# Kernel optimization log

Measured on AMD Instinct MI355X. Metric: run time of the kernel, lower is better.

## Reference

```python
import jax, jax.numpy as jnp
import numpy as np

N, K, D, H, DK, DV, L, E = 16384, 16, 128, 8, 16, 16, 2, 32
DFF = 4 * D
EPS = 1e-5


def _ln(x, g, b):
    mu = jnp.mean(x, axis=-1, keepdims=True)
    var = jnp.var(x, axis=-1, keepdims=True)
    return (x - mu) * jax.lax.rsqrt(var + EPS) * g + b


def setup_inputs() -> dict:
    key = jax.random.key(0)
    ks = jax.random.split(key, 20)
    inp = {
        "node_h": jax.random.normal(ks[0], (N, D), jnp.float32),
        "src_idx": jax.random.randint(ks[1], (N, K), 0, N),
        "edge_feat": jax.random.normal(ks[2], (N, K, E), jnp.float32),
        "t": jax.random.uniform(ks[3], (N, K), jnp.float32),
        "t_now": jnp.ones((1,), jnp.float32),
        # params (linear weights stored [in, out])
        "edge_fc_w": jax.random.normal(ks[4], (E, D), jnp.float32) * (2.0 / (E + D)) ** 0.5,
        "edge_fc_b": jnp.zeros((D,), jnp.float32),
        "basis_freq": jnp.asarray(1.0 / 10 ** np.linspace(0, 9, D), jnp.float32),
        "phase": jax.random.normal(ks[5], (D,), jnp.float32),
        "wq": jax.random.normal(ks[6], (L, D, H * DK), jnp.float32) * np.sqrt(2.0 / (D + DK)),
        "wk": jax.random.normal(ks[7], (L, D, H * DK), jnp.float32) * np.sqrt(2.0 / (D + DK)),
        "wv": jax.random.normal(ks[8], (L, D, H * DV), jnp.float32) * np.sqrt(2.0 / (D + DV)),
        "attn_fc_w": jax.random.normal(ks[9], (L, H * DV, D), jnp.float32) * (2.0 / (H * DV + D)) ** 0.5,
        "attn_fc_b": jnp.zeros((L, D), jnp.float32),
        "attn_ln_g": jnp.ones((L, D), jnp.float32),
        "attn_ln_b": jnp.zeros((L, D), jnp.float32),
        "ffn_w1": jax.random.normal(ks[10], (L, D, DFF), jnp.float32) * (1.0 / D) ** 0.5,
        "ffn_b1": jnp.zeros((L, DFF), jnp.float32),
        "ffn_w2": jax.random.normal(ks[11], (L, DFF, D), jnp.float32) * (1.0 / DFF) ** 0.5,
        "ffn_b2": jnp.zeros((L, D), jnp.float32),
        "ffn_ln_g": jnp.ones((L, D), jnp.float32),
        "ffn_ln_b": jnp.zeros((L, D), jnp.float32),
        "fea2node_w": jax.random.normal(ks[12], (D, D), jnp.float32) * (2.0 / (D + D)) ** 0.5,
        "fea2node_b": jnp.zeros((D,), jnp.float32),
        "final_ln_g": jnp.ones((D,), jnp.float32),
        "final_ln_b": jnp.zeros((D,), jnp.float32),
    }
    return inp


def reference(node_h, src_idx, edge_feat, t, t_now,
              edge_fc_w, edge_fc_b, basis_freq, phase,
              wq, wk, wv, attn_fc_w, attn_fc_b, attn_ln_g, attn_ln_b,
              ffn_w1, ffn_b1, ffn_w2, ffn_b2, ffn_ln_g, ffn_ln_b,
              fea2node_w, fea2node_b, final_ln_g, final_ln_b):
    scale = 1.0 / np.sqrt(DK).astype(np.float32)
    # message_func: gather src features, edge transform, temporal encoding
    t_enc = jnp.cos((t_now[0] - t)[..., None] * basis_freq + phase)        # [N,K,D]
    z = node_h[src_idx] + jax.nn.gelu(edge_feat @ edge_fc_w + edge_fc_b) + t_enc
    # reduce_func: inner_layer transformer blocks over the K-neighbor mailbox
    f = z
    for i in range(L):
        q = (f @ wq[i]).reshape(N, K, H, DK)
        k = (f @ wk[i]).reshape(N, K, H, DK)
        v = (f @ wv[i]).reshape(N, K, H, DV)
        attn = jax.nn.softmax(jnp.einsum('nqhd,nkhd->nhqk', q, k) * scale, axis=-1)
        out = jnp.einsum('nhqk,nkhd->nqhd', attn, v).reshape(N, K, H * DV)
        f = _ln(out @ attn_fc_w[i] + attn_fc_b[i] + f, attn_ln_g[i], attn_ln_b[i])
        hid = jax.nn.relu(f @ ffn_w1[i] + ffn_b1[i])                        # [N,K,4D]
        f = _ln(hid @ ffn_w2[i] + ffn_b2[i] + f, ffn_ln_g[i], ffn_ln_b[i])
    pooled = jnp.mean(f, axis=1)                                            # [N,D]
    out = _ln(jax.nn.gelu(pooled @ fea2node_w + fea2node_b) + node_h,
              final_ln_g, final_ln_b)
    return out
```

## Files before the change

### kernel.cpp

```cpp
#include <hip/hip_runtime.h>

#define NN 16384
#define OFF_EWT 0
#define OFF_WQT 4096
#define OFF_WKT 36864
#define OFF_WVT 69632
#define OFF_AFT 102400
#define OFF_W1T 135168
#define OFF_W2T 266240
#define OFF_F2N 397312
#define TOTAL_W 413696

typedef __attribute__((ext_vector_type(8))) short bf16x8;
typedef __attribute__((ext_vector_type(4))) short bf16x4;
typedef __attribute__((ext_vector_type(4))) float f32x4;

static __device__ __forceinline__ short f2bf(float f) {
  unsigned u = __builtin_bit_cast(unsigned, f);
  u += 0x7fffu + ((u >> 16) & 1u);
  return (short)(u >> 16);
}
static __device__ __forceinline__ float bf2f(short h) {
  unsigned u = ((unsigned)(unsigned short)h) << 16;
  return __builtin_bit_cast(float, u);
}
static __device__ __forceinline__ float gelu_f(float x) {
  float e = __expf(1.5957691216057308f * (x + 0.044715f * x * x * x));
  return x - x / (e + 1.0f);
}
static __device__ __forceinline__ f32x4 mfma16(bf16x8 a, bf16x8 b, f32x4 c) {
  return __builtin_amdgcn_mfma_f32_16x16x32_bf16(a, b, c, 0, 0, 0);
}
#define SWZM(row) (((((row) & 7) << 4)) ^ ((((row) >> 3) & 3) << 5))
static __device__ __forceinline__ int swzb(int row, int col) {
  return row * 256 + ((col * 2) ^ SWZM(row));
}
static __device__ __forceinline__ bf16x8 tile_ld8(const short* base, int row, int col) {
  return *(const bf16x8*)((const char*)base + swzb(row, col));
}
static __device__ __forceinline__ void tile_st16(short* base, int row, int col, short v) {
  *(short*)((char*)base + swzb(row, col)) = v;
}
static __device__ __forceinline__ void stage_w(short* dst, const short* src, int stride,
                                               int w, int lane) {
  #pragma unroll
  for (int it = 0; it < 2; ++it) {
    int dbase = (it * 4 + w) * 1024;
    int d = dbase + lane * 16;
    int row = d >> 8;
    int scolb = (d & 255) ^ SWZM(row);
    const short* sp = src + row * stride + (scolb >> 1);
    __builtin_amdgcn_global_load_lds(
        (const __attribute__((address_space(1))) unsigned int*)sp,
        (__attribute__((address_space(3))) unsigned int*)((char*)dst + dbase),
        16, 0, 0);
  }
}

#define LDS_FENCE() do {                                       \
    asm volatile("s_waitcnt lgkmcnt(0)" ::: "memory");         \
    __builtin_amdgcn_sched_barrier(0);                         \
  } while (0)

#define ISSUE(SRC, STRIDE) stage_w(bn, (SRC), (STRIDE), w, lane)
#define ENDSTEP() do {                                         \
    __syncthreads();                                           \
    short* _t = bc; bc = bn; bn = _t;                          \
  } while (0)

#define LD_FA2() do {                                                     \
    _Pragma("unroll") for (int _s = 0; _s < 4; ++_s) {                    \
      fA0[_s] = tile_ld8(myQ0, li, _s * 32 + lq * 8);                     \
      fA1[_s] = tile_ld8(myQ1, li, _s * 32 + lq * 8);                     \
    }                                                                     \
  } while (0)

#define ST_TILE(T, ACC)                                                   \
  _Pragma("unroll") for (int _c = 0; _c < 8; ++_c)                        \
    _Pragma("unroll") for (int _r = 0; _r < 4; ++_r)                      \
      tile_st16((T), lq * 4 + _r, _c * 16 + li, f2bf((ACC)[_c][_r]));

#define PROJ2D(BB)                                                        \
    f32x4 ga0 = F0, ga1 = F0, gb0 = F0, gb1 = F0;                         \
    _Pragma("unroll") for (int _s = 0; _s < 4; ++_s) {                    \
      int _sc = _s * 32 + lq * 8;                                         \
      bf16x8 _b0 = tile_ld8((BB), 0 + li, _sc);                           \
      bf16x8 _b1 = tile_ld8((BB), 16 + li, _sc);                          \
      ga0 = mfma16(fA0[_s], _b0, ga0); gb0 = mfma16(fA1[_s], _b0, gb0);   \
      ga1 = mfma16(fA0[_s], _b1, ga1); gb1 = mfma16(fA1[_s], _b1, gb1);   \
    }

#define ST2D(D0, D1, CB)                                                  \
    _Pragma("unroll") for (int _r = 0; _r < 4; ++_r) {                    \
      tile_st16((D0), lq * 4 + _r, (CB) * 16 + li, f2bf(ga0[_r]));        \
      tile_st16((D0), lq * 4 + _r, ((CB) + 1) * 16 + li, f2bf(ga1[_r]));  \
      tile_st16((D1), lq * 4 + _r, (CB) * 16 + li, f2bf(gb0[_r]));        \
      tile_st16((D1), lq * 4 + _r, ((CB) + 1) * 16 + li, f2bf(gb1[_r]));  \
    }

#define ACC2D(AR0, AR1, CB, BB)                                           \
    _Pragma("unroll") for (int _s = 0; _s < 4; ++_s) {                    \
      int _sc = _s * 32 + lq * 8;                                         \
      bf16x8 _b0 = tile_ld8((BB), 0 + li, _sc);                           \
      bf16x8 _b1 = tile_ld8((BB), 16 + li, _sc);                          \
      acc0[(CB)] = mfma16(AR0[_s], _b0, acc0[(CB)]);                      \
      acc1[(CB)] = mfma16(AR1[_s], _b0, acc1[(CB)]);                      \
      acc0[(CB) + 1] = mfma16(AR0[_s], _b1, acc0[(CB) + 1]);              \
      acc1[(CB) + 1] = mfma16(AR1[_s], _b1, acc1[(CB) + 1]);              \
    }

#define LAYER_NORM(A, GP, BP) do {                                        \
    float _gg[8], _bb[8];                                                 \
    _Pragma("unroll") for (int _c = 0; _c < 8; ++_c) {                    \
      _gg[_c] = (GP)[_c * 16 + li]; _bb[_c] = (BP)[_c * 16 + li]; }       \
    _Pragma("unroll") for (int _r = 0; _r < 4; ++_r) {                    \
      float _s1 = 0.f, _s2 = 0.f;                                         \
      _Pragma("unroll") for (int _c = 0; _c < 8; ++_c) {                  \
        float _v = (A)[_c][_r]; _s1 += _v; _s2 += _v * _v; }              \
      _Pragma("unroll") for (int _m = 1; _m <= 8; _m <<= 1) {             \
        _s1 += __shfl_xor(_s1, _m, 64); _s2 += __shfl_xor(_s2, _m, 64); } \
      float _mean = _s1 * (1.f / 128.f);                                  \
      float _var = _s2 * (1.f / 128.f) - _mean * _mean;                   \
      float _rstd = rsqrtf(_var + 1e-5f);                                 \
      _Pragma("unroll") for (int _c = 0; _c < 8; ++_c)                    \
        (A)[_c][_r] = ((A)[_c][_r] - _mean) * _rstd * _gg[_c] + _bb[_c];  \
    }                                                                     \
  } while (0)

#define ATTN(MYQ, MYK, VACC, OA) do {                                     \
    f32x4 _st[8];                                                         \
    _Pragma("unroll") for (int _h = 0; _h < 8; ++_h) {                    \
      bf16x8 _ka = B0, _qa = B0;                                          \
      if (lq < 2) {                                                       \
        _ka = tile_ld8((MYK), li, _h * 16 + lq * 8);                      \
        _qa = tile_ld8((MYQ), li, _h * 16 + lq * 8);                      \
      }                                                                   \
      _st[_h] = mfma16(_ka, _qa, F0);                                     \
    }                                                                     \
    LDS_FENCE();                                                          \
    _Pragma("unroll") for (int _c = 0; _c < 8; ++_c) {                    \
      bf16x4 _pk;                                                         \
      _Pragma("unroll") for (int _r = 0; _r < 4; ++_r)                    \
        _pk[_r] = f2bf((VACC)[_c][_r]);                                   \
      *(bf16x4*)((MYK) + (_c * 16 + li) * 16 + lq * 4) = _pk;             \
    }                                                                     \
    LDS_FENCE();                                                          \
    _Pragma("unroll") for (int _h = 0; _h < 8; ++_h) {                    \
      float _p[4]; float _mx = -1e30f;                                    \
      _Pragma("unroll") for (int _r = 0; _r < 4; ++_r) {                  \
        _p[_r] = _st[_h][_r] * 0.25f; _mx = fmaxf(_mx, _p[_r]); }         \
      _mx = fmaxf(_mx, __shfl_xor(_mx, 16, 64));                          \
      _mx = fmaxf(_mx, __shfl_xor(_mx, 32, 64));                          \
      float _sum = 0.f;                                                   \
      _Pragma("unroll") for (int _r = 0; _r < 4; ++_r) {                  \
        _p[_r] = __expf(_p[_r] - _mx); _sum += _p[_r]; }                  \
      _sum += __shfl_xor(_sum, 16, 64);                                   \
      _sum += __shfl_xor(_sum, 32, 64);                                   \
      float _inv = 1.0f / _sum;                                           \
      _Pragma("unroll") for (int _r = 0; _r < 4; ++_r) _p[_r] *= _inv;    \
      bf16x8 _pa;                                                         \
      _Pragma("unroll") for (int _j = 0; _j < 8; ++_j) {                  \
        float _v = __shfl(_p[_j & 3], li + 16 * (2 * lq + (_j >> 2)), 64);\
        _pa[_j] = (lq < 2) ? f2bf(_v) : (short)0;                         \
      }                                                                   \
      bf16x8 _vb = B0;                                                    \
      if (lq < 2) _vb = *(const bf16x8*)((MYK) + (_h * 16 + li) * 16 + lq * 8); \
      f32x4 _o = mfma16(_pa, _vb, F0);                                    \
      _Pragma("unroll") for (int _r = 0; _r < 4; ++_r)                    \
        tile_st16((MYQ), lq * 4 + _r, _h * 16 + li, f2bf(_o[_r]));        \
    }                                                                     \
    LDS_FENCE();                                                          \
    _Pragma("unroll") for (int _s = 0; _s < 4; ++_s)                      \
      (OA)[_s] = tile_ld8((MYQ), li, _s * 32 + lq * 8);                   \
  } while (0)

__global__ void prep_kernel(const float* __restrict__ ew, const float* __restrict__ wq,
                            const float* __restrict__ wk, const float* __restrict__ wv,
                            const float* __restrict__ afc, const float* __restrict__ w1,
                            const float* __restrict__ w2, const float* __restrict__ f2n,
                            short* __restrict__ wsb) {
  int tt = blockIdx.x * 256 + threadIdx.x;
  if (tt >= TOTAL_W) return;
  short v;
  if (tt < OFF_WQT) {
    int u = tt; int row = u >> 5, colr = u & 31;
    v = f2bf(ew[colr * 128 + row]);
  } else if (tt < OFF_WKT) {
    int u = tt - OFF_WQT; int i = u >> 14; u &= 16383; int row = u >> 7, colr = u & 127;
    v = f2bf(wq[i * 16384 + colr * 128 + row]);
  } else if (tt < OFF_WVT) {
    int u = tt - OFF_WKT; int i = u >> 14; u &= 16383; int row = u >> 7, colr = u & 127;
    v = f2bf(wk[i * 16384 + colr * 128 + row]);
  } else if (tt < OFF_AFT) {
    int u = tt - OFF_WVT; int i = u >> 14; u &= 16383; int row = u >> 7, colr = u & 127;
    v = f2bf(wv[i * 16384 + colr * 128 + row]);
  } else if (tt < OFF_W1T) {
    int u = tt - OFF_AFT; int i = u >> 14; u &= 16383; int row = u >> 7, colr = u & 127;
    v = f2bf(afc[i * 16384 + colr * 128 + row]);
  } else if (tt < OFF_W2T) {
    int u = tt - OFF_W1T; int i = u >> 16; u &= 65535; int row = u >> 7, colr = u & 127;
    v = f2bf(w1[i * 65536 + colr * 512 + row]);
  } else if (tt < OFF_F2N) {
    int u = tt - OFF_W2T; int i = u >> 16; u &= 65535; int row = u >> 9, colr = u & 511;
    v = f2bf(w2[i * 65536 + colr * 128 + row]);
  } else {
    int u = tt - OFF_F2N; int row = u >> 7, colr = u & 127;
    v = f2bf(f2n[colr * 128 + row]);
  }
  wsb[tt] = v;
}

__global__ __launch_bounds__(256, 2) void fused_kernel(
    const float* __restrict__ node_h, const int* __restrict__ src_idx,
    const float* __restrict__ edge_feat, const float* __restrict__ t_arr,
    const float* __restrict__ t_now, const float* __restrict__ edge_fc_b,
    const float* __restrict__ basis_freq, const float* __restrict__ phase,
    const float* __restrict__ attn_fc_b, const float* __restrict__ attn_ln_g,
    const float* __restrict__ attn_ln_b, const float* __restrict__ ffn_b1,
    const float* __restrict__ ffn_b2, const float* __restrict__ ffn_ln_g,
    const float* __restrict__ ffn_ln_b, const float* __restrict__ f2n_b,
    const float* __restrict__ fin_g, const float* __restrict__ fin_b,
    const short* __restrict__ wsb, float* __restrict__ out) {
  __shared__ __align__(16) short bufs0[4096];
  __shared__ __align__(16) short bufs1[4096];
  __shared__ __align__(16) short lds_qk[4][8192];

  const int tid = (int)threadIdx.x;
  const int w = tid >> 6, lane = tid & 63, li = lane & 15, lq = lane >> 4;
  const int n0 = (int)blockIdx.x * 8 + w * 2;
  const int n1 = n0 + 1;
  short* myQ0 = lds_qk[w];
  short* myK0 = lds_qk[w] + 2048;
  short* myQ1 = lds_qk[w] + 4096;
  short* myK1 = lds_qk[w] + 6144;
  short* bc = bufs0;
  short* bn = bufs1;
  const f32x4 F0 = {0.f, 0.f, 0.f, 0.f};
  const bf16x8 B0 = {0, 0, 0, 0, 0, 0, 0, 0};

  stage_w(bc, wsb + OFF_WQT, 128, w, lane);

  const float tnow = t_now[0];

  f32x4 acc0[8], acc1[8];
  {
    const short* ewt = wsb + OFF_EWT;
    const float* ef0 = edge_feat + ((size_t)(n0 * 16 + li)) * 32 + lq * 8;
    const float* ef1 = edge_feat + ((size_t)(n1 * 16 + li)) * 32 + lq * 8;
    f32x4 ea0 = *(const f32x4*)(ef0), ea0b = *(const f32x4*)(ef0 + 4);
    f32x4 ea1 = *(const f32x4*)(ef1), ea1b = *(const f32x4*)(ef1 + 4);
    bf16x8 e0, e1;
    #pragma unroll
    for (int j = 0; j < 4; ++j) {
      e0[j] = f2bf(ea0[j]); e0[j + 4] = f2bf(ea0b[j]);
      e1[j] = f2bf(ea1[j]); e1[j + 4] = f2bf(ea1b[j]);
    }
    #pragma unroll
    for (int c = 0; c < 8; ++c) {
      bf16x8 eb = *(const bf16x8*)(ewt + (c * 16 + li) * 32 + lq * 8);
      acc0[c] = mfma16(e0, eb, F0);
      acc1[c] = mfma16(e1, eb, F0);
    }
  }
  {
    float bfq[8], phs[8], ebs[8];
    #pragma unroll
    for (int c = 0; c < 8; ++c) {
      int col = c * 16 + li;
      bfq[c] = basis_freq[col]; phs[c] = phase[col]; ebs[c] = edge_fc_b[col];
    }
    #pragma unroll
    for (int r = 0; r < 4; ++r) {
      int m = lq * 4 + r;
      int s0 = src_idx[n0 * 16 + m], s1 = src_idx[n1 * 16 + m];
      float dt0 = tnow - t_arr[n0 * 16 + m], dt1 = tnow - t_arr[n1 * 16 + m];
      const float* nh0 = node_h + (size_t)s0 * 128;
      const float* nh1 = node_h + (size_t)s1 * 128;
      #pragma unroll
      for (int c = 0; c < 8; ++c) {
        int col = c * 16 + li;
        acc0[c][r] = gelu_f(acc0[c][r] + ebs[c]) + nh0[col] + __cosf(dt0 * bfq[c] + phs[c]);
        acc1[c][r] = gelu_f(acc1[c][r] + ebs[c]) + nh1[col] + __cosf(dt1 * bfq[c] + phs[c]);
      }
    }
  }
  ST_TILE(myQ0, acc0);
  ST_TILE(myQ1, acc1);
  __syncthreads();

  bf16x8 fA0[4], fA1[4];
  bf16x8 oa0_[4], oa1_[4];
  bf16x8 ha0_[4], ha1_[4];

  for (int il = 0; il < 2; ++il) {
    const short* WQT = wsb + OFF_WQT + il * 16384;
    const short* WKT = wsb + OFF_WKT + il * 16384;
    const short* WVT = wsb + OFF_WVT + il * 16384;
    const short* AFT = wsb + OFF_AFT + il * 16384;
    const short* W1T = wsb + OFF_W1T + il * 65536;
    const short* W2T = wsb + OFF_W2T + il * 65536;
    const short* WQN = wsb + OFF_WQT + ((il == 0) ? 16384 : 0);

    f32x4 vacc0[8], vacc1[8];

    #pragma unroll
    for (int q = 0; q < 4; ++q) {
      const short* nx = (q < 3) ? (WQT + (q + 1) * 4096) : WKT;
      ISSUE(nx, 128);
      if (q == 0) LD_FA2();
      { PROJ2D(bc); ST2D(myQ0, myQ1, q * 2); }
      ENDSTEP();
    }
    #pragma unroll
    for (int q = 0; q < 4; ++q) {
      const short* nx = (q < 3) ? (WKT + (q + 1) * 4096) : WVT;
      ISSUE(nx, 128);
      { PROJ2D(bc); ST2D(myK0, myK1, q * 2); }
      ENDSTEP();
    }
    #pragma unroll
    for (int q = 0; q < 4; ++q) {
      const short* nx = (q < 3) ? (WVT + (q + 1) * 4096) : AFT;
      ISSUE(nx, 128);
      {
        PROJ2D(bc);
        vacc0[q * 2] = ga0; vacc0[q * 2 + 1] = ga1;
        vacc1[q * 2] = gb0; vacc1[q * 2 + 1] = gb1;
      }
      if (q == 3) {
        ATTN(myQ0, myK0, vacc0, oa0_);
        ATTN(myQ1, myK1, vacc1, oa1_);
      }
      ENDSTEP();
    }
    #pragma unroll
    for (int q = 0; q < 4; ++q) {
      const short* nx = (q < 3) ? (AFT + (q + 1) * 4096) : W1T;
      ISSUE(nx, 128);
      #pragma unroll
      for (int j = 0; j < 2; ++j) {
        float b = attn_fc_b[il * 128 + (q * 2 + j) * 16 + li];
        #pragma unroll
        for (int r = 0; r < 4; ++r) { acc0[q * 2 + j][r] += b; acc1[q * 2 + j][r] += b; }
      }
      ACC2D(oa0_, oa1_, q * 2, bc);
      if (q == 3) {
        LAYER_NORM(acc0, attn_ln_g + il * 128, attn_ln_b + il * 128);
        LAYER_NORM(acc1, attn_ln_g + il * 128, attn_ln_b + il * 128);
        ST_TILE(myQ0, acc0);
        ST_TILE(myQ1, acc1);
        LD_FA2();
        #pragma unroll
        for (int c = 0; c < 8; ++c) {
          float b2 = ffn_b2[il * 128 + c * 16 + li];
          #pragma unroll
          for (int r = 0; r < 4; ++r) { acc0[c][r] += b2; acc1[c][r] += b2; }
        }
      }
      ENDSTEP();
    }

    for (int ct = 0; ct < 4; ++ct) {
      const short* W1c = W1T + ct * 16384;
      const short* W2c = W2T + ct * 128;
      const float* b1p = ffn_b1 + il * 512 + ct * 128;
      #pragma unroll
      for (int q = 0; q < 4; ++q) {
        const short* nx = (q < 3) ? (W1c + (q + 1) * 4096) : W2c;
        ISSUE(nx, (q < 3) ? 128 : 512);
        {
          PROJ2D(bc);
          float ba = b1p[(q * 2) * 16 + li], bb = b1p[(q * 2 + 1) * 16 + li];
          #pragma unroll
          for (int r = 0; r < 4; ++r) {
            tile_st16(myK0, lq * 4 + r, (q * 2) * 16 + li, f2bf(fmaxf(ga0[r] + ba, 0.f)));
            tile_st16(myK0, lq * 4 + r, (q * 2 + 1) * 16 + li, f2bf(fmaxf(ga1[r] + bb, 0.f)));
            tile_st16(myK1, lq * 4 + r, (q * 2) * 16 + li, f2bf(fmaxf(gb0[r] + ba, 0.f)));
            tile_st16(myK1, lq * 4 + r, (q * 2 + 1) * 16 + li, f2bf(fmaxf(gb1[r] + bb, 0.f)));
          }
        }
        if (q == 3) {
          LDS_FENCE();
          #pragma unroll
          for (int s = 0; s < 4; ++s) {
            ha0_[s] = tile_ld8(myK0, li, s * 32 + lq * 8);
            ha1_[s] = tile_ld8(myK1, li, s * 32 + lq * 8);
          }
        }
        ENDSTEP();
      }
      #pragma unroll
      for (int q = 0; q < 4; ++q) {
        const short* nx;
        int nstr;
        if (q < 3) { nx = W2c + (q + 1) * 32 * 512; nstr = 512; }
        else if (ct < 3) { nx = W1T + (ct + 1) * 16384; nstr = 128; }
        else { nx = WQN; nstr = 128; }
        ISSUE(nx, nstr);
        ACC2D(ha0_, ha1_, q * 2, bc);
        if (ct == 3 && q == 3) {
          LAYER_NORM(acc0, ffn_ln_g + il * 128, ffn_ln_b + il * 128);
          LAYER_NORM(acc1, ffn_ln_g + il * 128, ffn_ln_b + il * 128);
          ST_TILE(myQ0, acc0);
          ST_TILE(myQ1, acc1);
        }
        ENDSTEP();
      }
    }
  }
  asm volatile("s_waitcnt vmcnt(0)" ::: "memory");

  {
    float pc0[8], pc1[8];
    #pragma unroll
    for (int c = 0; c < 8; ++c) {
      float s0 = acc0[c][0] + acc0[c][1] + acc0[c][2] + acc0[c][3];
      float s1 = acc1[c][0] + acc1[c][1] + acc1[c][2] + acc1[c][3];
      s0 += __shfl_xor(s0, 16, 64); s0 += __shfl_xor(s0, 32, 64);
      s1 += __shfl_xor(s1, 16, 64); s1 += __shfl_xor(s1, 32, 64);
      pc0[c] = s0 * (1.f / 16.f);
      pc1[c] = s1 * (1.f / 16.f);
    }
    float* ps0 = (float*)myK0;
    float* ps1 = (float*)myK1;
    if (lq == 0) {
      #pragma unroll
      for (int c = 0; c < 8; ++c) { ps0[c * 16 + li] = pc0[c]; ps1[c * 16 + li] = pc1[c]; }
    }
    LDS_FENCE();
    const short* F2NT = wsb + OFF_F2N;
    #pragma unroll
    for (int nd = 0; nd < 2; ++nd) {
      const float* ps = nd ? ps1 : ps0;
      int n = nd ? n1 : n0;
      float yv[2];
      #pragma unroll
      for (int half = 0; half < 2; ++half) {
        int col = half * 64 + lane;
        float dot = 0.f;
        for (int d0 = 0; d0 < 128; d0 += 8) {
          bf16x8 wv8 = *(const bf16x8*)(F2NT + col * 128 + d0);
          f32x4 p0 = *(const f32x4*)(ps + d0);
          f32x4 p1 = *(const f32x4*)(ps + d0 + 4);
          dot += p0[0] * bf2f(wv8[0]) + p0[1] * bf2f(wv8[1]) + p0[2] * bf2f(wv8[2]) + p0[3] * bf2f(wv8[3]);
          dot += p1[0] * bf2f(wv8[4]) + p1[1] * bf2f(wv8[5]) + p1[2] * bf2f(wv8[6]) + p1[3] * bf2f(wv8[7]);
        }
        yv[half] = gelu_f(dot + f2n_b[col]) + node_h[(size_t)n * 128 + col];
      }
      float s1v = yv[0] + yv[1], s2v = yv[0] * yv[0] + yv[1] * yv[1];
      #pragma unroll
      for (int m = 1; m <= 32; m <<= 1) {
        s1v += __shfl_xor(s1v, m, 64); s2v += __shfl_xor(s2v, m, 64);
      }
      float mean = s1v * (1.f / 128.f);
      float var = s2v * (1.f / 128.f) - mean * mean;
      float rstd = rsqrtf(var + 1e-5f);
      #pragma unroll
      for (int half = 0; half < 2; ++half) {
        int col = half * 64 + lane;
        out[(size_t)n * 128 + col] = (yv[half] - mean) * rstd * fin_g[col] + fin_b[col];
      }
    }
  }
}

extern "C" void kernel_launch(void* const* d_in, const int* in_sizes, int n_in,
                              void* d_out, int out_size, void* d_ws, size_t ws_size,
                              hipStream_t stream) {
  const float* node_h    = (const float*)d_in[0];
  const int*   src_idx   = (const int*)d_in[1];
  const float* edge_feat = (const float*)d_in[2];
  const float* t_arr     = (const float*)d_in[3];
  const float* t_now     = (const float*)d_in[4];
  const float* edge_fc_w = (const float*)d_in[5];
  const float* edge_fc_b = (const float*)d_in[6];
  const float* basis_frq = (const float*)d_in[7];
  const float* phase     = (const float*)d_in[8];
  const float* wq        = (const float*)d_in[9];
  const float* wk        = (const float*)d_in[10];
  const float* wv        = (const float*)d_in[11];
  const float* attn_fc_w = (const float*)d_in[12];
  const float* attn_fc_b = (const float*)d_in[13];
  const float* attn_ln_g = (const float*)d_in[14];
  const float* attn_ln_b = (const float*)d_in[15];
  const float* ffn_w1    = (const float*)d_in[16];
  const float* ffn_b1    = (const float*)d_in[17];
  const float* ffn_w2    = (const float*)d_in[18];
  const float* ffn_b2    = (const float*)d_in[19];
  const float* ffn_ln_g  = (const float*)d_in[20];
  const float* ffn_ln_b  = (const float*)d_in[21];
  const float* f2n_w     = (const float*)d_in[22];
  const float* f2n_b     = (const float*)d_in[23];
  const float* fin_g     = (const float*)d_in[24];
  const float* fin_b     = (const float*)d_in[25];
  short* wsb = (short*)d_ws;

  prep_kernel<<<(TOTAL_W + 255) / 256, 256, 0, stream>>>(
      edge_fc_w, wq, wk, wv, attn_fc_w, ffn_w1, ffn_w2, f2n_w, wsb);
  fused_kernel<<<NN / 8, 256, 0, stream>>>(
      node_h, src_idx, edge_feat, t_arr, t_now, edge_fc_b, basis_frq, phase,
      attn_fc_b, attn_ln_g, attn_ln_b, ffn_b1, ffn_b2, ffn_ln_g, ffn_ln_b,
      f2n_b, fin_g, fin_b, wsb, (float*)d_out);
}
```

Before: 689.7 us.

## Process one node per wave instead of two to raise occupancy

Each wave now handles a single node's 16-neighbor mailbox rather than two. This halves accumulator registers and per-wave LDS, allows three blocks per CU via launch bounds, and doubles the grid size. The cost is that each staged weight tile feeds half as many MFMAs, so weight staging traffic and block-level barriers per node double. An extra LDS fence is added before attention.

Result: slower. 801.3 us (+16.2%).

```diff
diff --git a/kernel.cpp b/kernel.cpp
--- a/kernel.cpp
+++ b/kernel.cpp
@@ -68,45 +68,38 @@
     short* _t = bc; bc = bn; bn = _t;                          \
   } while (0)
 
-#define LD_FA2() do {                                                     \
-    _Pragma("unroll") for (int _s = 0; _s < 4; ++_s) {                    \
-      fA0[_s] = tile_ld8(myQ0, li, _s * 32 + lq * 8);                     \
-      fA1[_s] = tile_ld8(myQ1, li, _s * 32 + lq * 8);                     \
-    }                                                                     \
-  } while (0)
+#define LD_FA(SRC)                                                        \
+  _Pragma("unroll") for (int _s = 0; _s < 4; ++_s)                        \
+      fA[_s] = tile_ld8((SRC), li, _s * 32 + lq * 8);
 
 #define ST_TILE(T, ACC)                                                   \
   _Pragma("unroll") for (int _c = 0; _c < 8; ++_c)                        \
     _Pragma("unroll") for (int _r = 0; _r < 4; ++_r)                      \
       tile_st16((T), lq * 4 + _r, _c * 16 + li, f2bf((ACC)[_c][_r]));
 
-#define PROJ2D(BB)                                                        \
-    f32x4 ga0 = F0, ga1 = F0, gb0 = F0, gb1 = F0;                         \
+#define PROJ1(BB)                                                         \
+    f32x4 g0 = F0, g1 = F0;                                               \
     _Pragma("unroll") for (int _s = 0; _s < 4; ++_s) {                    \
       int _sc = _s * 32 + lq * 8;                                         \
       bf16x8 _b0 = tile_ld8((BB), 0 + li, _sc);                           \
       bf16x8 _b1 = tile_ld8((BB), 16 + li, _sc);                          \
-      ga0 = mfma16(fA0[_s], _b0, ga0); gb0 = mfma16(fA1[_s], _b0, gb0);   \
-      ga1 = mfma16(fA0[_s], _b1, ga1); gb1 = mfma16(fA1[_s], _b1, gb1);   \
-    }
-
-#define ST2D(D0, D1, CB)                                                  \
+      g0 = mfma16(fA[_s], _b0, g0);                                       \
+      g1 = mfma16(fA[_s], _b1, g1);                                       \
+    }
+
+#define ST1(DST, CB)                                                      \
     _Pragma("unroll") for (int _r = 0; _r < 4; ++_r) {                    \
-      tile_st16((D0), lq * 4 + _r, (CB) * 16 + li, f2bf(ga0[_r]));        \
-      tile_st16((D0), lq * 4 + _r, ((CB) + 1) * 16 + li, f2bf(ga1[_r]));  \
-      tile_st16((D1), lq * 4 + _r, (CB) * 16 + li, f2bf(gb0[_r]));        \
-      tile_st16((D1), lq * 4 + _r, ((CB) + 1) * 16 + li, f2bf(gb1[_r]));  \
-    }
-
-#define ACC2D(AR0, AR1, CB, BB)                                           \
+      tile_st16((DST), lq * 4 + _r, (CB) * 16 + li, f2bf(g0[_r]));        \
+      tile_st16((DST), lq * 4 + _r, ((CB) + 1) * 16 + li, f2bf(g1[_r]));  \
+    }
+
+#define ACC1(AR, CB, BB)                                                  \
     _Pragma("unroll") for (int _s = 0; _s < 4; ++_s) {                    \
       int _sc = _s * 32 + lq * 8;                                         \
       bf16x8 _b0 = tile_ld8((BB), 0 + li, _sc);                           \
       bf16x8 _b1 = tile_ld8((BB), 16 + li, _sc);                          \
-      acc0[(CB)] = mfma16(AR0[_s], _b0, acc0[(CB)]);                      \
-      acc1[(CB)] = mfma16(AR1[_s], _b0, acc1[(CB)]);                      \
-      acc0[(CB) + 1] = mfma16(AR0[_s], _b1, acc0[(CB) + 1]);              \
-      acc1[(CB) + 1] = mfma16(AR1[_s], _b1, acc1[(CB) + 1]);              \
+      acc[(CB)] = mfma16(AR[_s], _b0, acc[(CB)]);                         \
+      acc[(CB) + 1] = mfma16(AR[_s], _b1, acc[(CB) + 1]);                 \
     }
 
 #define LAYER_NORM(A, GP, BP) do {                                        \
@@ -210,7 +203,7 @@
   wsb[tt] = v;
 }
 
-__global__ __launch_bounds__(256, 2) void fused_kernel(
+__global__ __launch_bounds__(256, 3) void fused_kernel(
     const float* __restrict__ node_h, const int* __restrict__ src_idx,
     const float* __restrict__ edge_feat, const float* __restrict__ t_arr,
     const float* __restrict__ t_now, const float* __restrict__ edge_fc_b,
@@ -223,16 +216,13 @@
     const short* __restrict__ wsb, float* __restrict__ out) {
   __shared__ __align__(16) short bufs0[4096];
   __shared__ __align__(16) short bufs1[4096];
-  __shared__ __align__(16) short lds_qk[4][8192];
+  __shared__ __align__(16) short lds_qk[4][4096];
 
   const int tid = (int)threadIdx.x;
   const int w = tid >> 6, lane = tid & 63, li = lane & 15, lq = lane >> 4;
-  const int n0 = (int)blockIdx.x * 8 + w * 2;
-  const int n1 = n0 + 1;
-  short* myQ0 = lds_qk[w];
-  short* myK0 = lds_qk[w] + 2048;
-  short* myQ1 = lds_qk[w] + 4096;
-  short* myK1 = lds_qk[w] + 6144;
+  const int n = (int)blockIdx.x * 4 + w;
+  short* myQ = lds_qk[w];
+  short* myK = lds_qk[w] + 2048;
   short* bc = bufs0;
   short* bn = bufs1;
   const f32x4 F0 = {0.f, 0.f, 0.f, 0.f};
@@ -242,24 +232,19 @@
 
   const float tnow = t_now[0];
 
-  f32x4 acc0[8], acc1[8];
+  f32x4 acc[8];
   {
+    const float* ef = edge_feat + ((size_t)(n * 16 + li)) * 32 + lq * 8;
+    f32x4 e0 = *(const f32x4*)(ef);
+    f32x4 e1 = *(const f32x4*)(ef + 4);
+    bf16x8 ea;
+    #pragma unroll
+    for (int j = 0; j < 4; ++j) { ea[j] = f2bf(e0[j]); ea[j + 4] = f2bf(e1[j]); }
     const short* ewt = wsb + OFF_EWT;
-    const float* ef0 = edge_feat + ((size_t)(n0 * 16 + li)) * 32 + lq * 8;
-    const float* ef1 = edge_feat + ((size_t)(n1 * 16 + li)) * 32 + lq * 8;
-    f32x4 ea0 = *(const f32x4*)(ef0), ea0b = *(const f32x4*)(ef0 + 4);
-    f32x4 ea1 = *(const f32x4*)(ef1), ea1b = *(const f32x4*)(ef1 + 4);
-    bf16x8 e0, e1;
-    #pragma unroll
-    for (int j = 0; j < 4; ++j) {
-      e0[j] = f2bf(ea0[j]); e0[j + 4] = f2bf(ea0b[j]);
-      e1[j] = f2bf(ea1[j]); e1[j + 4] = f2bf(ea1b[j]);
-    }
     #pragma unroll
     for (int c = 0; c < 8; ++c) {
       bf16x8 eb = *(const bf16x8*)(ewt + (c * 16 + li) * 32 + lq * 8);
-      acc0[c] = mfma16(e0, eb, F0);
-      acc1[c] = mfma16(e1, eb, F0);
+      acc[c] = mfma16(ea, eb, F0);
     }
   }
   {
@@ -272,25 +257,25 @@
     #pragma unroll
     for (int r = 0; r < 4; ++r) {
       int m = lq * 4 + r;
-      int s0 = src_idx[n0 * 16 + m], s1 = src_idx[n1 * 16 + m];
-      float dt0 = tnow - t_arr[n0 * 16 + m], dt1 = tnow - t_arr[n1 * 16 + m];
-      const float* nh0 = node_h + (size_t)s0 * 128;
-      const float* nh1 = node_h + (size_t)s1 * 128;
+      int sidx = src_idx[n * 16 + m];
+      float dt = tnow - t_arr[n * 16 + m];
+      const float* nh = node_h + (size_t)sidx * 128;
       #pragma unroll
       for (int c = 0; c < 8; ++c) {
         int col = c * 16 + li;
-        acc0[c][r] = gelu_f(acc0[c][r] + ebs[c]) + nh0[col] + __cosf(dt0 * bfq[c] + phs[c]);
-        acc1[c][r] = gelu_f(acc1[c][r] + ebs[c]) + nh1[col] + __cosf(dt1 * bfq[c] + phs[c]);
-      }
-    }
-  }
-  ST_TILE(myQ0, acc0);
-  ST_TILE(myQ1, acc1);
+        float x = gelu_f(acc[c][r] + ebs[c]);
+        x += nh[col];
+        x += __cosf(dt * bfq[c] + phs[c]);
+        acc[c][r] = x;
+      }
+    }
+  }
+  ST_TILE(myQ, acc);
   __syncthreads();
 
-  bf16x8 fA0[4], fA1[4];
-  bf16x8 oa0_[4], oa1_[4];
-  bf16x8 ha0_[4], ha1_[4];
+  bf16x8 fA[4];
+  bf16x8 oa_[4];
+  bf16x8 ha_[4];
 
   for (int il = 0; il < 2; ++il) {
     const short* WQT = wsb + OFF_WQT + il * 16384;
@@ -301,37 +286,34 @@
     const short* W2T = wsb + OFF_W2T + il * 65536;
     const short* WQN = wsb + OFF_WQT + ((il == 0) ? 16384 : 0);
 
-    f32x4 vacc0[8], vacc1[8];
-
     #pragma unroll
     for (int q = 0; q < 4; ++q) {
       const short* nx = (q < 3) ? (WQT + (q + 1) * 4096) : WKT;
       ISSUE(nx, 128);
-      if (q == 0) LD_FA2();
-      { PROJ2D(bc); ST2D(myQ0, myQ1, q * 2); }
+      if (q == 0) LD_FA(myQ);
+      { PROJ1(bc); ST1(myQ, q * 2); }
       ENDSTEP();
     }
     #pragma unroll
     for (int q = 0; q < 4; ++q) {
       const short* nx = (q < 3) ? (WKT + (q + 1) * 4096) : WVT;
       ISSUE(nx, 128);
-      { PROJ2D(bc); ST2D(myK0, myK1, q * 2); }
+      { PROJ1(bc); ST1(myK, q * 2); }
       ENDSTEP();
     }
-    #pragma unroll
-    for (int q = 0; q < 4; ++q) {
-      const short* nx = (q < 3) ? (WVT + (q + 1) * 4096) : AFT;
-      ISSUE(nx, 128);
-      {
-        PROJ2D(bc);
-        vacc0[q * 2] = ga0; vacc0[q * 2 + 1] = ga1;
-        vacc1[q * 2] = gb0; vacc1[q * 2 + 1] = gb1;
-      }
-      if (q == 3) {
-        ATTN(myQ0, myK0, vacc0, oa0_);
-        ATTN(myQ1, myK1, vacc1, oa1_);
-      }
-      ENDSTEP();
+    {
+      f32x4 vacc[8];
+      #pragma unroll
+      for (int q = 0; q < 4; ++q) {
+        const short* nx = (q < 3) ? (WVT + (q + 1) * 4096) : AFT;
+        ISSUE(nx, 128);
+        { PROJ1(bc); vacc[q * 2] = g0; vacc[q * 2 + 1] = g1; }
+        if (q == 3) {
+          LDS_FENCE();
+          ATTN(myQ, myK, vacc, oa_);
+        }
+        ENDSTEP();
+      }
     }
     #pragma unroll
     for (int q = 0; q < 4; ++q) {
@@ -341,20 +323,18 @@
       for (int j = 0; j < 2; ++j) {
         float b = attn_fc_b[il * 128 + (q * 2 + j) * 16 + li];
         #pragma unroll
-        for (int r = 0; r < 4; ++r) { acc0[q * 2 + j][r] += b; acc1[q * 2 + j][r] += b; }
-      }
-      ACC2D(oa0_, oa1_, q * 2, bc);
+        for (int r = 0; r < 4; ++r) acc[q * 2 + j][r] += b;
+      }
+      ACC1(oa_, q * 2, bc);
       if (q == 3) {
-        LAYER_NORM(acc0, attn_ln_g + il * 128, attn_ln_b + il * 128);
-        LAYER_NORM(acc1, attn_ln_g + il * 128, attn_ln_b + il * 128);
-        ST_TILE(myQ0, acc0);
-        ST_TILE(myQ1, acc1);
-        LD_FA2();
+        LAYER_NORM(acc, attn_ln_g + il * 128, attn_ln_b + il * 128);
+        ST_TILE(myQ, acc);
+        LD_FA(myQ);
         #pragma unroll
         for (int c = 0; c < 8; ++c) {
           float b2 = ffn_b2[il * 128 + c * 16 + li];
           #pragma unroll
-          for (int r = 0; r < 4; ++r) { acc0[c][r] += b2; acc1[c][r] += b2; }
+          for (int r = 0; r < 4; ++r) acc[c][r] += b2;
         }
       }
       ENDSTEP();
@@ -369,23 +349,18 @@
         const short* nx = (q < 3) ? (W1c + (q + 1) * 4096) : W2c;
         ISSUE(nx, (q < 3) ? 128 : 512);
         {
-          PROJ2D(bc);
+          PROJ1(bc);
           float ba = b1p[(q * 2) * 16 + li], bb = b1p[(q * 2 + 1) * 16 + li];
           #pragma unroll
           for (int r = 0; r < 4; ++r) {
-            tile_st16(myK0, lq * 4 + r, (q * 2) * 16 + li, f2bf(fmaxf(ga0[r] + ba, 0.f)));
-            tile_st16(myK0, lq * 4 + r, (q * 2 + 1) * 16 + li, f2bf(fmaxf(ga1[r] + bb, 0.f)));
-            tile_st16(myK1, lq * 4 + r, (q * 2) * 16 + li, f2bf(fmaxf(gb0[r] + ba, 0.f)));
-            tile_st16(myK1, lq * 4 + r, (q * 2 + 1) * 16 + li, f2bf(fmaxf(gb1[r] + bb, 0.f)));
+            tile_st16(myK, lq * 4 + r, (q * 2) * 16 + li, f2bf(fmaxf(g0[r] + ba, 0.f)));
+            tile_st16(myK, lq * 4 + r, (q * 2 + 1) * 16 + li, f2bf(fmaxf(g1[r] + bb, 0.f)));
           }
         }
         if (q == 3) {
           LDS_FENCE();
           #pragma unroll
-          for (int s = 0; s < 4; ++s) {
-            ha0_[s] = tile_ld8(myK0, li, s * 32 + lq * 8);
-            ha1_[s] = tile_ld8(myK1, li, s * 32 + lq * 8);
-          }
+          for (int s = 0; s < 4; ++s) ha_[s] = tile_ld8(myK, li, s * 32 + lq * 8);
         }
         ENDSTEP();
       }
@@ -397,12 +372,10 @@
         else if (ct < 3) { nx = W1T + (ct + 1) * 16384; nstr = 128; }
         else { nx = WQN; nstr = 128; }
         ISSUE(nx, nstr);
-        ACC2D(ha0_, ha1_, q * 2, bc);
+        ACC1(ha_, q * 2, bc);
         if (ct == 3 && q == 3) {
-          LAYER_NORM(acc0, ffn_ln_g + il * 128, ffn_ln_b + il * 128);
-          LAYER_NORM(acc1, ffn_ln_g + il * 128, ffn_ln_b + il * 128);
-          ST_TILE(myQ0, acc0);
-          ST_TILE(myQ1, acc1);
+          LAYER_NORM(acc, ffn_ln_g + il * 128, ffn_ln_b + il * 128);
+          ST_TILE(myQ, acc);
         }
         ENDSTEP();
       }
@@ -410,57 +383,45 @@
   }
   asm volatile("s_waitcnt vmcnt(0)" ::: "memory");
 
-  {
-    float pc0[8], pc1[8];
-    #pragma unroll
-    for (int c = 0; c < 8; ++c) {
-      float s0 = acc0[c][0] + acc0[c][1] + acc0[c][2] + acc0[c][3];
-      float s1 = acc1[c][0] + acc1[c][1] + acc1[c][2] + acc1[c][3];
-      s0 += __shfl_xor(s0, 16, 64); s0 += __shfl_xor(s0, 32, 64);
-      s1 += __shfl_xor(s1, 16, 64); s1 += __shfl_xor(s1, 32, 64);
-      pc0[c] = s0 * (1.f / 16.f);
-      pc1[c] = s1 * (1.f / 16.f);
-    }
-    float* ps0 = (float*)myK0;
-    float* ps1 = (float*)myK1;
-    if (lq == 0) {
-      #pragma unroll
-      for (int c = 0; c < 8; ++c) { ps0[c * 16 + li] = pc0[c]; ps1[c * 16 + li] = pc1[c]; }
-    }
-    LDS_FENCE();
-    const short* F2NT = wsb + OFF_F2N;
-    #pragma unroll
-    for (int nd = 0; nd < 2; ++nd) {
-      const float* ps = nd ? ps1 : ps0;
-      int n = nd ? n1 : n0;
-      float yv[2];
-      #pragma unroll
-      for (int half = 0; half < 2; ++half) {
-        int col = half * 64 + lane;
-        float dot = 0.f;
-        for (int d0 = 0; d0 < 128; d0 += 8) {
-          bf16x8 wv8 = *(const bf16x8*)(F2NT + col * 128 + d0);
-          f32x4 p0 = *(const f32x4*)(ps + d0);
-          f32x4 p1 = *(const f32x4*)(ps + d0 + 4);
-          dot += p0[0] * bf2f(wv8[0]) + p0[1] * bf2f(wv8[1]) + p0[2] * bf2f(wv8[2]) + p0[3] * bf2f(wv8[3]);
-          dot += p1[0] * bf2f(wv8[4]) + p1[1] * bf2f(wv8[5]) + p1[2] * bf2f(wv8[6]) + p1[3] * bf2f(wv8[7]);
-        }
-        yv[half] = gelu_f(dot + f2n_b[col]) + node_h[(size_t)n * 128 + col];
-      }
-      float s1v = yv[0] + yv[1], s2v = yv[0] * yv[0] + yv[1] * yv[1];
-      #pragma unroll
-      for (int m = 1; m <= 32; m <<= 1) {
-        s1v += __shfl_xor(s1v, m, 64); s2v += __shfl_xor(s2v, m, 64);
-      }
-      float mean = s1v * (1.f / 128.f);
-      float var = s2v * (1.f / 128.f) - mean * mean;
-      float rstd = rsqrtf(var + 1e-5f);
-      #pragma unroll
-      for (int half = 0; half < 2; ++half) {
-        int col = half * 64 + lane;
-        out[(size_t)n * 128 + col] = (yv[half] - mean) * rstd * fin_g[col] + fin_b[col];
-      }
-    }
+  float pc[8];
+  #pragma unroll
+  for (int c = 0; c < 8; ++c) {
+    float s = acc[c][0] + acc[c][1] + acc[c][2] + acc[c][3];
+    s += __shfl_xor(s, 16, 64);
+    s += __shfl_xor(s, 32, 64);
+    pc[c] = s * (1.f / 16.f);
+  }
+  float* ps = (float*)myK;
+  if (lq == 0) {
+    #pragma unroll
+    for (int c = 0; c < 8; ++c) ps[c * 16 + li] = pc[c];
+  }
+  LDS_FENCE();
+  const short* F2NT = wsb + OFF_F2N;
+  float yv[2];
+  #pragma unroll
+  for (int half = 0; half < 2; ++half) {
+    int col = half * 64 + lane;
+    float dot = 0.f;
+    for (int d0 = 0; d0 < 128; d0 += 8) {
+      bf16x8 wv8 = *(const bf16x8*)(F2NT + col * 128 + d0);
+      f32x4 p0 = *(const f32x4*)(ps + d0);
+      f32x4 p1 = *(const f32x4*)(ps + d0 + 4);
+      dot += p0[0] * bf2f(wv8[0]) + p0[1] * bf2f(wv8[1]) + p0[2] * bf2f(wv8[2]) + p0[3] * bf2f(wv8[3]);
+      dot += p1[0] * bf2f(wv8[4]) + p1[1] * bf2f(wv8[5]) + p1[2] * bf2f(wv8[6]) + p1[3] * bf2f(wv8[7]);
+    }
+    yv[half] = gelu_f(dot + f2n_b[col]) + node_h[(size_t)n * 128 + col];
+  }
+  float s1 = yv[0] + yv[1], s2 = yv[0] * yv[0] + yv[1] * yv[1];
+  #pragma unroll
+  for (int m = 1; m <= 32; m <<= 1) { s1 += __shfl_xor(s1, m, 64); s2 += __shfl_xor(s2, m, 64); }
+  float mean = s1 * (1.f / 128.f);
+  float var = s2 * (1.f / 128.f) - mean * mean;
+  float rstd = rsqrtf(var + 1e-5f);
+  #pragma unroll
+  for (int half = 0; half < 2; ++half) {
+    int col = half * 64 + lane;
+    out[(size_t)n * 128 + col] = (yv[half] - mean) * rstd * fin_g[col] + fin_b[col];
   }
 }
 
@@ -497,7 +458,7 @@
 
   prep_kernel<<<(TOTAL_W + 255) / 256, 256, 0, stream>>>(
       edge_fc_w, wq, wk, wv, attn_fc_w, ffn_w1, ffn_w2, f2n_w, wsb);
-  fused_kernel<<<NN / 8, 256, 0, stream>>>(
+  fused_kernel<<<NN / 4, 256, 0, stream>>>(
       node_h, src_idx, edge_feat, t_arr, t_now, edge_fc_b, basis_frq, phase,
       attn_fc_b, attn_ln_g, attn_ln_b, ffn_b1, ffn_b2, ffn_ln_g, ffn_ln_b,
       f2n_b, fin_g, fin_b, wsb, (float*)d_out);
```
